# Performance work log

Measured on AMD Instinct MI355X. Metric: run time of the kernel, lower is better.

The kernel has to match this reference:

```python
import jax, jax.numpy as jnp
import numpy as np
from jax import lax

B, T, C, K = 16, 1024, 512, 5
PAD = (K - 1) // 2
EPS_LN = 1e-5
EPS_BN = 1e-5


def setup_inputs() -> dict:
    key = jax.random.key(0)
    ks = jax.random.split(key, 8)
    s1 = 1.0 / np.sqrt(C)          # fan-in of pointwise conv1 (C -> 2C)
    s2 = 1.0 / np.sqrt(2 * C * K)  # fan-in of k=5 conv (2C -> 2C)
    s3 = 1.0 / np.sqrt(C)          # fan-in of pointwise conv3 (C -> C)
    return {
        "x": jax.random.normal(ks[0], (B, T, C), jnp.float32),
        "ln_g": jnp.ones((C,), jnp.float32),
        "ln_b": jnp.zeros((C,), jnp.float32),
        "w1": (jax.random.normal(ks[1], (2 * C, C), jnp.float32) * s1),
        "b1": jnp.zeros((2 * C,), jnp.float32),
        "w2": (jax.random.normal(ks[2], (K, 2 * C, 2 * C), jnp.float32) * s2),  # WIO layout
        "b2": jnp.zeros((2 * C,), jnp.float32),
        "bn_g": jnp.ones((C,), jnp.float32),
        "bn_b": jnp.zeros((C,), jnp.float32),
        "bn_mean": jax.random.normal(ks[3], (C,), jnp.float32) * 0.1,
        "bn_var": jax.random.uniform(ks[4], (C,), jnp.float32, 0.5, 1.5),
        "w3": (jax.random.normal(ks[5], (C, C), jnp.float32) * s3),
        "b3": jnp.zeros((C,), jnp.float32),
    }


def reference(x, ln_g, ln_b, w1, b1, w2, b2, bn_g, bn_b, bn_mean, bn_var, w3, b3):
    # LayerNorm over channel dim (B, T, C)
    mu = jnp.mean(x, axis=-1, keepdims=True)
    var = jnp.mean(jnp.square(x - mu), axis=-1, keepdims=True)
    h = (x - mu) * lax.rsqrt(var + EPS_LN) * ln_g + ln_b

    # pointwise conv C -> 2C (kernel 1 == GEMM), then Swish
    h = jnp.einsum('btc,oc->bto', h, w1) + b1        # (B, T, 2C)
    h = h * jax.nn.sigmoid(h)

    # kernel-5 conv 2C -> 2C, 'same' padding, channels-last
    h = lax.conv_general_dilated(
        h, w2, window_strides=(1,), padding=[(PAD, PAD)],
        dimension_numbers=('NWC', 'WIO', 'NWC')) + b2  # (B, T, 2C)

    # GLU over channel dim: first half * sigmoid(second half)
    a, g = h[..., :C], h[..., C:]
    h = a * jax.nn.sigmoid(g)                        # (B, T, C)

    # BatchNorm1d(C), eval mode (running stats)
    h = (h - bn_mean) * lax.rsqrt(bn_var + EPS_BN) * bn_g + bn_b

    # pointwise conv C -> C; dropout is identity at inference.
    # Torch output is sequential(...)(B,C,T).transpose(1,2) -> (B, T, C)
    return jnp.einsum('btc,oc->bto', h, w3) + b3
```

## Files before the change

### kernel.cpp

```cpp
#include <hip/hip_runtime.h>
#include <cstdint>


#define NB    16
#define TT    1024
#define CC    512
#define C2    1024
#define TPAD  1028

typedef unsigned short u16;
typedef short bf16x8 __attribute__((ext_vector_type(8)));
typedef float f32x4  __attribute__((ext_vector_type(4)));
typedef __attribute__((address_space(3))) u16 lds_u16;
typedef const __attribute__((address_space(1))) u16 glb_u16;

__device__ __forceinline__ float bf2f(u16 u) {
  union { unsigned int i; float f; } v; v.i = ((unsigned int)u) << 16; return v.f;
}
__device__ __forceinline__ u16 f2bf(float f) {
  union { float f; unsigned int i; } v; v.f = f;
  unsigned int x = v.i;
  return (u16)((x + 0x7fffu + ((x >> 16) & 1u)) >> 16);
}

__global__ __launch_bounds__(256) void prep_k(
    const float* __restrict__ w1, u16* __restrict__ w1b,
    const float* __restrict__ w3, u16* __restrict__ w3b,
    u16* __restrict__ h1p) {
  const int b = blockIdx.x;
  if (b < 512) {
    const int i = (b * 256 + threadIdx.x) * 4;
    float4 v = *(const float4*)(w1 + i);
    u16 o[4] = { f2bf(v.x), f2bf(v.y), f2bf(v.z), f2bf(v.w) };
    *(uint2*)(w1b + i) = *(const uint2*)o;
  } else if (b < 768) {
    const int i = ((b - 512) * 256 + threadIdx.x) * 4;
    float4 v = *(const float4*)(w3 + i);
    u16 o[4] = { f2bf(v.x), f2bf(v.y), f2bf(v.z), f2bf(v.w) };
    *(uint2*)(w3b + i) = *(const uint2*)o;
  } else {
    const int idx = (b - 768) * 256 + threadIdx.x;
    const int bb  = idx >> 9;
    const int rem = idx & 511;
    const int ri  = rem >> 7;
    const int c8  = (rem & 127) * 8;
    const int row = bb * TPAD + (ri < 2 ? ri : 1024 + ri);
    uint4 z = make_uint4(0u, 0u, 0u, 0u);
    *(uint4*)(h1p + (size_t)row * C2 + c8) = z;
  }
}

__global__ void transpose_w2(const float* __restrict__ w2, u16* __restrict__ w2t) {
  __shared__ u16 t[64][65];
  const int k  = blockIdx.z;
  const int i0 = blockIdx.x * 64, o0 = blockIdx.y * 64;
  const int tx = threadIdx.x, ty = threadIdx.y;
  for (int r = ty; r < 64; r += 4)
    t[r][tx] = f2bf(w2[((size_t)(k * C2) + i0 + r) * C2 + o0 + tx]);
  __syncthreads();
  for (int r = ty; r < 64; r += 4)
    w2t[((size_t)(k * C2) + o0 + r) * C2 + i0 + tx] = t[tx][r];
}

__global__ __launch_bounds__(256) void layernorm_k(
    const float* __restrict__ x, const float* __restrict__ lng,
    const float* __restrict__ lnb, u16* __restrict__ out) {
  const int tok  = blockIdx.x * 4 + (threadIdx.x >> 6);
  const int lane = threadIdx.x & 63;
  const float* xp = x + (size_t)tok * CC + lane * 8;
  float f[8];
  *(float4*)(f)     = *(const float4*)(xp);
  *(float4*)(f + 4) = *(const float4*)(xp + 4);
  float s = 0.f, s2 = 0.f;
#pragma unroll
  for (int j = 0; j < 8; j++) { s += f[j]; s2 += f[j] * f[j]; }
#pragma unroll
  for (int m = 32; m >= 1; m >>= 1) { s += __shfl_xor(s, m, 64); s2 += __shfl_xor(s2, m, 64); }
  const float mu  = s  * (1.f / 512.f);
  const float var = s2 * (1.f / 512.f) - mu * mu;
  const float rs  = rsqrtf(var + 1e-5f);
  u16 ov[8];
#pragma unroll
  for (int j = 0; j < 8; j++) {
    const int c = lane * 8 + j;
    ov[j] = f2bf((f[j] - mu) * rs * lng[c] + lnb[c]);
  }
  *(uint4*)(out + (size_t)tok * CC + lane * 8) = *(const uint4*)ov;
}

template <int EPI>
__global__ __launch_bounds__(256, 3) void gemm_bt(
    const u16* __restrict__ A, const u16* __restrict__ Bt,
    const float* __restrict__ bias, void* __restrict__ outv,
    const int Kd, const int ldA) {
  __shared__ __align__(16) u16 smem[20480];
  const int tid  = threadIdx.x;
  const int m0   = blockIdx.x * 128;
  const int n0   = blockIdx.y * 128;
  const int wave = tid >> 6, lane = tid & 63;
  const int wm = (wave & 1) * 64, wn = (wave >> 1) * 64;
  const int quad = lane >> 4, l16 = lane & 15;
  const int row = tid >> 2;
  const int kc  = (tid & 3) * 8;
  const int J = Kd >> 5;

  const u16* Ap0 = A + (size_t)(m0 + row) * ldA + kc;
  const u16* Ap1 = Ap0 + (size_t)64 * ldA;
  const u16* Bp0 = Bt + (size_t)(n0 + row) * Kd + kc;
  const u16* Bp1 = Bp0 + (size_t)64 * Kd;

  f32x4 acc[4][4] = {};
  uint4 rA0 = *(const uint4*)Ap0, rA1 = *(const uint4*)Ap1;
  uint4 rB0 = *(const uint4*)Bp0, rB1 = *(const uint4*)Bp1;
  *(uint4*)(smem + row * 40 + kc)                = rA0;
  *(uint4*)(smem + (64 + row) * 40 + kc)         = rA1;
  *(uint4*)(smem + 10240 + row * 40 + kc)        = rB0;
  *(uint4*)(smem + 10240 + (64 + row) * 40 + kc) = rB1;
  rA0 = *(const uint4*)(Ap0 + 32); rA1 = *(const uint4*)(Ap1 + 32);
  rB0 = *(const uint4*)(Bp0 + 32); rB1 = *(const uint4*)(Bp1 + 32);
  __syncthreads();

#pragma unroll 1
  for (int j = 0; j < J; j++) {
    const u16* curA = smem + (j & 1) * 5120;
    const u16* curB = smem + 10240 + (j & 1) * 5120;
    if (j + 1 < J) {
      u16* nxtA = smem + ((j + 1) & 1) * 5120;
      u16* nxtB = smem + 10240 + ((j + 1) & 1) * 5120;
      *(uint4*)(nxtA + row * 40 + kc)        = rA0;
      *(uint4*)(nxtA + (64 + row) * 40 + kc) = rA1;
      *(uint4*)(nxtB + row * 40 + kc)        = rB0;
      *(uint4*)(nxtB + (64 + row) * 40 + kc) = rB1;
    }
    {
      const int k2 = (j + 2 < J) ? (j + 2) * 32 : 0;
      rA0 = *(const uint4*)(Ap0 + k2); rA1 = *(const uint4*)(Ap1 + k2);
      rB0 = *(const uint4*)(Bp0 + k2); rB1 = *(const uint4*)(Bp1 + k2);
    }
    bf16x8 af[4], bfr[4];
#pragma unroll
    for (int i = 0; i < 4; i++)
      af[i] = *(const bf16x8*)(curA + (wm + i * 16 + l16) * 40 + quad * 8);
#pragma unroll
    for (int i = 0; i < 4; i++)
      bfr[i] = *(const bf16x8*)(curB + (wn + i * 16 + l16) * 40 + quad * 8);
#pragma unroll
    for (int mi = 0; mi < 4; mi++)
#pragma unroll
      for (int ni = 0; ni < 4; ni++)
        acc[mi][ni] = __builtin_amdgcn_mfma_f32_16x16x32_bf16(
            af[mi], bfr[ni], acc[mi][ni], 0, 0, 0);
    __syncthreads();
  }

  float bv[4];
#pragma unroll
  for (int ni = 0; ni < 4; ni++) bv[ni] = bias[n0 + wn + ni * 16 + l16];

  if (EPI == 0) {
    u16* epi = smem + wave * 4608;
#pragma unroll
    for (int mi = 0; mi < 4; mi++)
#pragma unroll
      for (int ni = 0; ni < 4; ni++)
#pragma unroll
        for (int r = 0; r < 4; r++) {
          float v = acc[mi][ni][r] + bv[ni];
          v = v / (1.f + __expf(-v));
          epi[(mi * 16 + quad * 4 + r) * 72 + ni * 16 + l16] = f2bf(v);
        }
    u16* h1p = (u16*)outv;
#pragma unroll
    for (int p = 0; p < 8; p++) {
      const int rrow = p * 8 + (lane >> 3);
      const int colb = (lane & 7) * 8;
      uint4 v = *(const uint4*)(epi + rrow * 72 + colb);
      const int rr = m0 + wm + rrow;
      const int bb = rr >> 10, tt = rr & 1023;
      *(uint4*)(h1p + (size_t)(bb * TPAD + tt + 2) * C2 + n0 + wn + colb) = v;
    }
  } else {
    float* fepi = (float*)(smem + wave * 4608);
    float* outf = (float*)outv;
#pragma unroll
    for (int mi = 0; mi < 4; mi++) {
      float* fp = fepi + (mi & 1) * 1088;
#pragma unroll
      for (int ni = 0; ni < 4; ni++)
#pragma unroll
        for (int r = 0; r < 4; r++)
          fp[(quad * 4 + r) * 68 + ni * 16 + l16] = acc[mi][ni][r] + bv[ni];
#pragma unroll
      for (int p = 0; p < 4; p++) {
        const int rrow = p * 4 + (lane >> 4);
        const int col  = (lane & 15) * 4;
        float4 v = *(const float4*)(fp + rrow * 68 + col);
        *(float4*)(outf + (size_t)(m0 + wm + mi * 16 + rrow) * CC + n0 + wn + col) = v;
      }
    }
  }
}

__global__ __launch_bounds__(256, 2) void conv5_mfma(
    const u16* __restrict__ h1p, const u16* __restrict__ w2t,
    const float* __restrict__ b2, u16* __restrict__ out) {
  __shared__ __align__(16) u16 smem[30880];
  const int tid = threadIdx.x;
  const int mt  = blockIdx.x;
  const int n0  = blockIdx.y * 128;
  const int bb  = mt >> 2;
  const int t0  = (mt & 3) * 256;
  const size_t arow0 = (size_t)bb * TPAD + t0;
  const int wave = tid >> 6, lane = tid & 63;
  const int wm = (wave & 1) * 128, wn = (wave >> 1) * 64;
  const int quad = lane >> 4, l16 = lane & 15;
  const int row = tid >> 2;
  const int kc  = (tid & 3) * 8;
  u16* lsB = smem + 10400;

  const u16* Ap0 = h1p + (arow0 + row) * C2 + kc;
  const u16* Ap1 = Ap0 + (size_t)64 * C2;
  const u16* Ap2 = Ap0 + (size_t)128 * C2;
  const u16* Ap3 = Ap0 + (size_t)192 * C2;
  const u16* Ap4 = h1p + (arow0 + 256 + row) * C2 + kc;

  const u16* Bb0 = w2t + (size_t)(n0 + wave * 16 + (lane & 15)) * C2 + (lane >> 4) * 8;
  const u16* Bb1 = Bb0 + (size_t)64 * C2;

  f32x4 acc[8][4] = {};
  uint4 rA0, rA1, rA2, rA3, rA4;

#define BG(PTR, T5, GQ, I0)                                                    \
  __builtin_amdgcn_global_load_lds(                                            \
      (glb_u16*)((PTR) + (size_t)(T5) * C2 * C2 + (I0)),                       \
      (lds_u16*)(lsB + ((T5) * 8 + (GQ)) * 512), 16, 0, 0);

  rA0 = *(const uint4*)Ap0; rA1 = *(const uint4*)Ap1;
  rA2 = *(const uint4*)Ap2; rA3 = *(const uint4*)Ap3;
  if (tid < 16) rA4 = *(const uint4*)Ap4;

#pragma unroll 1
  for (int j = 0; j < 32; j++) {
    __syncthreads();
    {
      const int ib0 = j * 32;
#pragma unroll
      for (int t5 = 0; t5 < 5; t5++) {
        BG(Bb0, t5, wave, ib0)
        BG(Bb1, t5, wave + 4, ib0)
      }
    }
    *(uint4*)(smem + row * 40 + kc)         = rA0;
    *(uint4*)(smem + (64 + row) * 40 + kc)  = rA1;
    *(uint4*)(smem + (128 + row) * 40 + kc) = rA2;
    *(uint4*)(smem + (192 + row) * 40 + kc) = rA3;
    if (tid < 16) *(uint4*)(smem + (256 + row) * 40 + kc) = rA4;
    __syncthreads();
    {
      const int ia = (j + 1 < 32) ? (j + 1) * 32 : 0;
      rA0 = *(const uint4*)(Ap0 + ia);
      rA1 = *(const uint4*)(Ap1 + ia);
      rA2 = *(const uint4*)(Ap2 + ia);
      rA3 = *(const uint4*)(Ap3 + ia);
      if (tid < 16) rA4 = *(const uint4*)(Ap4 + ia);
    }
#pragma unroll
    for (int k = 0; k < 5; k++) {
      bf16x8 bfr[4];
#pragma unroll
      for (int i = 0; i < 4; i++)
        bfr[i] = *(const bf16x8*)(lsB + (k * 8 + (wn >> 4) + i) * 512 + lane * 8);
#pragma unroll
      for (int h = 0; h < 2; h++) {
        bf16x8 af[4];
#pragma unroll
        for (int i = 0; i < 4; i++)
          af[i] = *(const bf16x8*)(smem + (wm + (h * 4 + i) * 16 + l16 + k) * 40 + quad * 8);
#pragma unroll
        for (int mi = 0; mi < 4; mi++)
#pragma unroll
          for (int ni = 0; ni < 4; ni++)
            acc[h * 4 + mi][ni] = __builtin_amdgcn_mfma_f32_16x16x32_bf16(
                af[mi], bfr[ni], acc[h * 4 + mi][ni], 0, 0, 0);
      }
    }
  }
#undef BG
  __syncthreads();

  float bv[4];
#pragma unroll
  for (int ni = 0; ni < 4; ni++) bv[ni] = b2[n0 + wn + ni * 16 + l16];

  u16* epi = smem + wave * 4608;
  const size_t orow0 = (size_t)bb * TT + t0;
#pragma unroll
  for (int h = 0; h < 2; h++) {
#pragma unroll
    for (int mi = 0; mi < 4; mi++)
#pragma unroll
      for (int ni = 0; ni < 4; ni++)
#pragma unroll
        for (int r = 0; r < 4; r++)
          epi[(mi * 16 + quad * 4 + r) * 72 + ni * 16 + l16] =
              f2bf(acc[h * 4 + mi][ni][r] + bv[ni]);
#pragma unroll
    for (int p = 0; p < 8; p++) {
      const int rrow = p * 8 + (lane >> 3);
      const int colb = (lane & 7) * 8;
      uint4 v = *(const uint4*)(epi + rrow * 72 + colb);
      *(uint4*)(out + (orow0 + wm + h * 64 + rrow) * C2 + n0 + wn + colb) = v;
    }
  }
}

__global__ __launch_bounds__(256) void glu_bn_k(
    const u16* __restrict__ hc, const float* __restrict__ bg,
    const float* __restrict__ bb_, const float* __restrict__ bm,
    const float* __restrict__ bv, u16* __restrict__ out) {
  const int idx = blockIdx.x * 256 + threadIdx.x;
  const int r  = idx >> 6;
  const int c8 = (idx & 63) * 8;
  const u16* pa = hc + (size_t)r * C2 + c8;
  uint4 ra = *(const uint4*)pa;
  uint4 rg = *(const uint4*)(pa + CC);
  u16 av[8], gv[8], ov[8];
  *(uint4*)av = ra; *(uint4*)gv = rg;
#pragma unroll
  for (int j = 0; j < 8; j++) {
    const int c = c8 + j;
    const float a = bf2f(av[j]);
    const float g = bf2f(gv[j]);
    const float h = a / (1.f + __expf(-g));
    const float sc = bg[c] * rsqrtf(bv[c] + 1e-5f);
    ov[j] = f2bf((h - bm[c]) * sc + bb_[c]);
  }
  *(uint4*)(out + (size_t)r * CC + c8) = *(const uint4*)ov;
}

extern "C" void kernel_launch(void* const* d_in, const int* in_sizes, int n_in,
                              void* d_out, int out_size, void* d_ws, size_t ws_size,
                              hipStream_t stream) {
  const float* x   = (const float*)d_in[0];
  const float* lng = (const float*)d_in[1];
  const float* lnb = (const float*)d_in[2];
  const float* w1  = (const float*)d_in[3];
  const float* b1  = (const float*)d_in[4];
  const float* w2  = (const float*)d_in[5];
  const float* b2  = (const float*)d_in[6];
  const float* bng = (const float*)d_in[7];
  const float* bnb = (const float*)d_in[8];
  const float* bnm = (const float*)d_in[9];
  const float* bnv = (const float*)d_in[10];
  const float* w3  = (const float*)d_in[11];
  const float* b3  = (const float*)d_in[12];

  u16* ws  = (u16*)d_ws;
  u16* hln = ws;
  u16* h2  = hln;
  u16* h1p = ws + 8388608;
  u16* w2t = h1p + 16842752;
  u16* hcv = w2t + 5242880;
  u16* w1b = hcv + 16777216;
  u16* w3b = w1b + 524288;

  prep_k      <<<800, 256, 0, stream>>>(w1, w1b, w3, w3b, h1p);
  transpose_w2<<<dim3(16, 16, 5), dim3(64, 4), 0, stream>>>(w2, w2t);
  layernorm_k <<<4096, 256, 0, stream>>>(x, lng, lnb, hln);
  gemm_bt<0>  <<<dim3(128, 8), 256, 0, stream>>>(hln, w1b, b1, h1p, 512, 512);
  conv5_mfma  <<<dim3(64, 8), 256, 0, stream>>>(h1p, w2t, b2, hcv);
  glu_bn_k    <<<4096, 256, 0, stream>>>(hcv, bng, bnb, bnm, bnv, h2);
  gemm_bt<1>  <<<dim3(128, 4), 256, 0, stream>>>(h2, w3b, b3, d_out, 512, 512);
}
```

Measured before the change: 321.2 us.

## Fuse GLU and BatchNorm into conv5 epilogue by pairing gate channel tiles

The conv5 kernel's N tile now covers 64 'a' channels and the matching 64 gate channels (offset by 512), not 128 contiguous outputs. This lets the epilogue apply GLU and eval-mode BatchNorm directly and write the C-wide h2 tensor. The separate glu_bn kernel and the full 2C-wide intermediate write and read go away. In exchange the epilogue stages results in LDS over two passes with extra barriers and does the sigmoid math inside the GEMM kernel.

```diff
diff --git a/kernel.cpp b/kernel.cpp
--- a/kernel.cpp
+++ b/kernel.cpp
@@ -203,11 +203,14 @@
 
 __global__ __launch_bounds__(256, 2) void conv5_mfma(
     const u16* __restrict__ h1p, const u16* __restrict__ w2t,
-    const float* __restrict__ b2, u16* __restrict__ out) {
+    const float* __restrict__ b2,
+    const float* __restrict__ bng, const float* __restrict__ bnb,
+    const float* __restrict__ bnm, const float* __restrict__ bnv,
+    u16* __restrict__ h2) {
   __shared__ __align__(16) u16 smem[30880];
   const int tid = threadIdx.x;
   const int mt  = blockIdx.x;
-  const int n0  = blockIdx.y * 128;
+  const int ya  = blockIdx.y * 64;
   const int bb  = mt >> 2;
   const int t0  = (mt & 3) * 256;
   const size_t arow0 = (size_t)bb * TPAD + t0;
@@ -224,8 +227,8 @@
   const u16* Ap3 = Ap0 + (size_t)192 * C2;
   const u16* Ap4 = h1p + (arow0 + 256 + row) * C2 + kc;
 
-  const u16* Bb0 = w2t + (size_t)(n0 + wave * 16 + (lane & 15)) * C2 + (lane >> 4) * 8;
-  const u16* Bb1 = Bb0 + (size_t)64 * C2;
+  const u16* Bb0 = w2t + (size_t)(ya + wave * 16 + (lane & 15)) * C2 + (lane >> 4) * 8;
+  const u16* Bb1 = w2t + (size_t)(512 + ya + wave * 16 + (lane & 15)) * C2 + (lane >> 4) * 8;
 
   f32x4 acc[8][4] = {};
   uint4 rA0, rA1, rA2, rA3, rA4;
@@ -290,52 +293,54 @@
 
   float bv[4];
 #pragma unroll
-  for (int ni = 0; ni < 4; ni++) bv[ni] = b2[n0 + wn + ni * 16 + l16];
-
-  u16* epi = smem + wave * 4608;
+  for (int ni = 0; ni < 4; ni++)
+    bv[ni] = b2[(wn >> 6) * 512 + ya + ni * 16 + l16];
+
+  const int cb8 = (lane & 7) * 8;
+  float sc8[8], bm8[8], bb8[8];
+#pragma unroll
+  for (int jj = 0; jj < 8; jj++) {
+    const int c = ya + cb8 + jj;
+    sc8[jj] = bng[c] * rsqrtf(bnv[c] + 1e-5f);
+    bm8[jj] = bnm[c];
+    bb8[jj] = bnb[c];
+  }
+
+  u16* abuf = smem;
+  u16* gbuf = smem + 9216;
   const size_t orow0 = (size_t)bb * TT + t0;
-#pragma unroll
-  for (int h = 0; h < 2; h++) {
-#pragma unroll
-    for (int mi = 0; mi < 4; mi++)
-#pragma unroll
-      for (int ni = 0; ni < 4; ni++)
-#pragma unroll
-        for (int r = 0; r < 4; r++)
-          epi[(mi * 16 + quad * 4 + r) * 72 + ni * 16 + l16] =
-              f2bf(acc[h * 4 + mi][ni][r] + bv[ni]);
-#pragma unroll
-    for (int p = 0; p < 8; p++) {
-      const int rrow = p * 8 + (lane >> 3);
-      const int colb = (lane & 7) * 8;
-      uint4 v = *(const uint4*)(epi + rrow * 72 + colb);
-      *(uint4*)(out + (orow0 + wm + h * 64 + rrow) * C2 + n0 + wn + colb) = v;
-    }
-  }
-}
-
-__global__ __launch_bounds__(256) void glu_bn_k(
-    const u16* __restrict__ hc, const float* __restrict__ bg,
-    const float* __restrict__ bb_, const float* __restrict__ bm,
-    const float* __restrict__ bv, u16* __restrict__ out) {
-  const int idx = blockIdx.x * 256 + threadIdx.x;
-  const int r  = idx >> 6;
-  const int c8 = (idx & 63) * 8;
-  const u16* pa = hc + (size_t)r * C2 + c8;
-  uint4 ra = *(const uint4*)pa;
-  uint4 rg = *(const uint4*)(pa + CC);
-  u16 av[8], gv[8], ov[8];
-  *(uint4*)av = ra; *(uint4*)gv = rg;
-#pragma unroll
-  for (int j = 0; j < 8; j++) {
-    const int c = c8 + j;
-    const float a = bf2f(av[j]);
-    const float g = bf2f(gv[j]);
-    const float h = a / (1.f + __expf(-g));
-    const float sc = bg[c] * rsqrtf(bv[c] + 1e-5f);
-    ov[j] = f2bf((h - bm[c]) * sc + bb_[c]);
-  }
-  *(uint4*)(out + (size_t)r * CC + c8) = *(const uint4*)ov;
+#pragma unroll 1
+  for (int hh = 0; hh < 2; hh++) {
+    if ((wave & 1) == hh) {
+      u16* buf = (wn >> 6) ? gbuf : abuf;
+#pragma unroll
+      for (int mi = 0; mi < 8; mi++)
+#pragma unroll
+        for (int ni = 0; ni < 4; ni++)
+#pragma unroll
+          for (int r = 0; r < 4; r++)
+            buf[(mi * 16 + quad * 4 + r) * 72 + ni * 16 + l16] =
+                f2bf(acc[mi][ni][r] + bv[ni]);
+    }
+    __syncthreads();
+#pragma unroll
+    for (int p = 0; p < 4; p++) {
+      const int rr = wave * 32 + p * 8 + (lane >> 3);
+      uint4 va = *(const uint4*)(abuf + rr * 72 + cb8);
+      uint4 vg = *(const uint4*)(gbuf + rr * 72 + cb8);
+      u16 aa[8], gg[8], oo[8];
+      *(uint4*)aa = va; *(uint4*)gg = vg;
+#pragma unroll
+      for (int jj = 0; jj < 8; jj++) {
+        const float a = bf2f(aa[jj]);
+        const float g = bf2f(gg[jj]);
+        const float h = a / (1.f + __expf(-g));
+        oo[jj] = f2bf((h - bm8[jj]) * sc8[jj] + bb8[jj]);
+      }
+      *(uint4*)(h2 + (orow0 + hh * 128 + rr) * CC + ya + cb8) = *(const uint4*)oo;
+    }
+    __syncthreads();
+  }
 }
 
 extern "C" void kernel_launch(void* const* d_in, const int* in_sizes, int n_in,
@@ -368,7 +373,6 @@
   transpose_w2<<<dim3(16, 16, 5), dim3(64, 4), 0, stream>>>(w2, w2t);
   layernorm_k <<<4096, 256, 0, stream>>>(x, lng, lnb, hln);
   gemm_bt<0>  <<<dim3(128, 8), 256, 0, stream>>>(hln, w1b, b1, h1p, 512, 512);
-  conv5_mfma  <<<dim3(64, 8), 256, 0, stream>>>(h1p, w2t, b2, hcv);
-  glu_bn_k    <<<4096, 256, 0, stream>>>(hcv, bng, bnb, bnm, bnv, h2);
+  conv5_mfma  <<<dim3(64, 8), 256, 0, stream>>>(h1p, w2t, b2, bng, bnb, bnm, bnv, h2);
   gemm_bt<1>  <<<dim3(128, 4), 256, 0, stream>>>(h2, w3b, b3, d_out, 512, 512);
 }
```

Result: faster. 310.3 us (-3.4%).
